# Kernel optimization log

Hardware: AMD Instinct MI355X
Metric: run time of the kernel (lower is better)

Reference implementation:

```python
import jax, jax.numpy as jnp
import numpy as np

B, C, H, W = 8, 256, 64, 64
G = min(C // 4, 32)  # 32 groups, as in the torch module
EPS = 1e-6


def setup_inputs() -> dict:
    key = jax.random.key(0)
    ks = jax.random.split(key, 12)
    s = 1.0 / np.sqrt(C)
    inp = {
        "x": jax.random.normal(ks[0], (B, C, H, W), jnp.float32),
        "gn_scale": 1.0 + 0.02 * jax.random.normal(ks[1], (C,), jnp.float32),
        "gn_bias": 0.02 * jax.random.normal(ks[2], (C,), jnp.float32),
        "w_q": s * jax.random.normal(ks[3], (C, C), jnp.float32),
        "b_q": 0.01 * jax.random.normal(ks[4], (C,), jnp.float32),
        "w_k": s * jax.random.normal(ks[5], (C, C), jnp.float32),
        "b_k": 0.01 * jax.random.normal(ks[6], (C,), jnp.float32),
        "w_v": s * jax.random.normal(ks[7], (C, C), jnp.float32),
        "b_v": 0.01 * jax.random.normal(ks[8], (C,), jnp.float32),
        "w_o": s * jax.random.normal(ks[9], (C, C), jnp.float32),
        "b_o": 0.01 * jax.random.normal(ks[10], (C,), jnp.float32),
    }
    return inp


def _group_norm(x, scale, bias):
    b, c, h, w = x.shape
    xg = x.reshape(b, G, c // G, h, w)
    m = jnp.mean(xg, axis=(2, 3, 4), keepdims=True)
    v = jnp.var(xg, axis=(2, 3, 4), keepdims=True)
    xn = ((xg - m) * jax.lax.rsqrt(v + EPS)).reshape(b, c, h, w)
    return xn * scale[None, :, None, None] + bias[None, :, None, None]


def _nin(h, w, b):
    # 1x1 conv: [B,C,H,W] x [out,in] -> [B,out,H,W]
    return jnp.einsum('bchw,oc->bohw', h, w) + b[None, :, None, None]


def reference(x, gn_scale, gn_bias, w_q, b_q, w_k, b_k, w_v, b_v, w_o, b_o):
    b, c, h, w = x.shape
    n = h * w
    hn = _group_norm(x, gn_scale, gn_bias)
    q = _nin(hn, w_q, b_q).reshape(b, c, n)
    k = _nin(hn, w_k, b_k).reshape(b, c, n)
    v = _nin(hn, w_v, b_v).reshape(b, c, n)
    scale = jnp.asarray(c, x.dtype) ** -0.5
    att = jax.nn.softmax(jnp.einsum('bcn,bcm->bnm', q, k) * scale, axis=-1)
    out = jnp.einsum('bnm,bcm->bcn', att, v).reshape(b, c, h, w)
    out = _nin(out, w_o, b_o)
    return (x + out) / jnp.asarray(np.sqrt(2.0), x.dtype)
```

## Files before the change

### kernel.cpp

```cpp
#include <hip/hip_runtime.h>

typedef __attribute__((ext_vector_type(8))) short bf16x8;
typedef __attribute__((ext_vector_type(4))) float f32x4;
typedef unsigned short us;

#define MFMA(a, b, c) __builtin_amdgcn_mfma_f32_16x16x32_bf16((a), (b), (c), 0, 0, 0)

__device__ __forceinline__ us f2bf(float f) {
  union { float f; unsigned int u; } x; x.f = f;
  return (us)((x.u + 0x7FFFu + ((x.u >> 16) & 1u)) >> 16);
}

__device__ __forceinline__ void glds16(const us* g, us* l) {
  __builtin_amdgcn_global_load_lds(
      (const __attribute__((address_space(1))) unsigned int*)g,
      (__attribute__((address_space(3))) unsigned int*)l, 16, 0, 0);
}

__global__ __launch_bounds__(256) void conv_w(const float* __restrict__ a, const float* __restrict__ b,
                                              const float* __restrict__ c, const float* __restrict__ d,
                                              us* __restrict__ oa, us* __restrict__ ob,
                                              us* __restrict__ oc, us* __restrict__ od) {
  int i = blockIdx.x * 256 + threadIdx.x;
  oa[i] = f2bf(a[i]); ob[i] = f2bf(b[i]); oc[i] = f2bf(c[i]); od[i] = f2bf(d[i]);
}

__global__ __launch_bounds__(256) void gn_kernel(const float* __restrict__ x,
                                                 const float* __restrict__ scale,
                                                 const float* __restrict__ bias,
                                                 us* __restrict__ hnT) {
  int b = blockIdx.y, g = blockIdx.x;
  int tid = threadIdx.x;
  int c0 = g * 8;
  const float* xb = x + (((size_t)b * 256 + c0) << 12);
  float s = 0.f, sq = 0.f;
  for (int j = 0; j < 8; ++j) {
    const float* xc = xb + ((size_t)j << 12);
    for (int n = tid; n < 4096; n += 256) {
      float v = xc[n];
      s += v; sq += v * v;
    }
  }
  for (int off = 32; off; off >>= 1) { s += __shfl_xor(s, off); sq += __shfl_xor(sq, off); }
  __shared__ float red[8];
  int w = tid >> 6, lane = tid & 63;
  if (lane == 0) { red[w] = s; red[4 + w] = sq; }
  __syncthreads();
  s  = red[0] + red[1] + red[2] + red[3];
  sq = red[4] + red[5] + red[6] + red[7];
  float mean = s * (1.f / 32768.f);
  float var  = sq * (1.f / 32768.f) - mean * mean;
  float rstd = rsqrtf(var + 1e-6f);
  float aa[8], bb[8];
  for (int j = 0; j < 8; ++j) {
    float sc = scale[c0 + j] * rstd;
    aa[j] = sc; bb[j] = bias[c0 + j] - mean * sc;
  }
  us* dst = hnT + ((size_t)b << 12) * 256 + c0;
  for (int n = tid; n < 4096; n += 256) {
    union { us u16[8]; uint4 v; } t;
    for (int j = 0; j < 8; ++j) {
      float v = xb[((size_t)j << 12) + n];
      t.u16[j] = f2bf(v * aa[j] + bb[j]);
    }
    *(uint4*)(dst + (size_t)n * 256) = t.v;
  }
}

__global__ __launch_bounds__(256) void proj_nk(const us* __restrict__ hnT,
                                               const us* __restrict__ wq, const us* __restrict__ wk,
                                               const float* __restrict__ bq, const float* __restrict__ bk,
                                               us* __restrict__ qT, us* __restrict__ kT) {
  __shared__ us A_s[128 * 64];
  __shared__ us B_s[128 * 64];
  int bx = blockIdx.x, by = blockIdx.y;
  int tid = threadIdx.x, w = tid >> 6, lane = tid & 63;
  int l15 = lane & 15, quad = lane >> 4;
  const us* wsrc; const float* bsrc; us* dst; int o0;
  if (by < 2) { wsrc = wq; bsrc = bq; dst = qT; o0 = by * 128; }
  else        { wsrc = wk; bsrc = bk; dst = kT; o0 = (by - 2) * 128; }
  size_t R0 = (size_t)bx * 128;
  int wm = (w & 1) * 64, wn = (w >> 1) * 64;
  f32x4 z = {0.f, 0.f, 0.f, 0.f};
  f32x4 acc[4][4] = {{z,z,z,z},{z,z,z,z},{z,z,z,z},{z,z,z,z}};

  for (int kk = 0; kk < 256; kk += 64) {
    __syncthreads();
#pragma unroll
    for (int j = 0; j < 4; ++j) {
      int cidx = j * 256 + tid;
      int row = cidx >> 3, cc = cidx & 7;
      int gch = (cc ^ (row & 7)) * 8;
      glds16(hnT + (R0 + row) * 256 + kk + gch, A_s + cidx * 8);
      glds16(wsrc + (size_t)(o0 + row) * 256 + kk + gch, B_s + cidx * 8);
    }
    __syncthreads();
#pragma unroll
    for (int k2 = 0; k2 < 2; ++k2) {
      int ch = (k2 * 4 + quad) ^ (l15 & 7);
      bf16x8 af[4], bf[4];
#pragma unroll
      for (int i = 0; i < 4; ++i) {
        af[i] = *(const bf16x8*)(A_s + (wm + i * 16 + l15) * 64 + ch * 8);
        bf[i] = *(const bf16x8*)(B_s + (wn + i * 16 + l15) * 64 + ch * 8);
      }
#pragma unroll
      for (int i = 0; i < 4; ++i)
#pragma unroll
        for (int j = 0; j < 4; ++j)
          acc[i][j] = MFMA(af[i], bf[j], acc[i][j]);
    }
  }
#pragma unroll
  for (int j = 0; j < 4; ++j) {
    int o = o0 + wn + j * 16 + l15;
    float bv = bsrc[o];
#pragma unroll
    for (int i = 0; i < 4; ++i)
#pragma unroll
      for (int r = 0; r < 4; ++r)
        dst[(R0 + wm + i * 16 + quad * 4 + r) * 256 + o] = f2bf(acc[i][j][r] + bv);
  }
}

__global__ __launch_bounds__(256) void proj_cn(const us* __restrict__ A,
                                               const us* __restrict__ Bm,
                                               const float* __restrict__ bias,
                                               const float* __restrict__ x,
                                               float* __restrict__ outf,
                                               us* __restrict__ outb, int mode) {
  __shared__ us A_s[128 * 64];
  __shared__ us B_s[128 * 64];
  int bx = blockIdx.x, bb = blockIdx.y;
  int mt = bx & 1, ntile = bx >> 1;
  int tid = threadIdx.x, w = tid >> 6, lane = tid & 63;
  int l15 = lane & 15, quad = lane >> 4;
  int R0 = mt * 128;
  size_t NB = (size_t)bb * 4096 + ntile * 128;
  int wm = (w & 1) * 64, wn = (w >> 1) * 64;
  f32x4 z = {0.f, 0.f, 0.f, 0.f};
  f32x4 acc[4][4] = {{z,z,z,z},{z,z,z,z},{z,z,z,z},{z,z,z,z}};

  for (int kk = 0; kk < 256; kk += 64) {
    __syncthreads();
#pragma unroll
    for (int j = 0; j < 4; ++j) {
      int cidx = j * 256 + tid;
      int row = cidx >> 3, cc = cidx & 7;
      int gch = (cc ^ (row & 7)) * 8;
      glds16(A + (size_t)(R0 + row) * 256 + kk + gch, A_s + cidx * 8);
      glds16(Bm + (NB + row) * 256 + kk + gch, B_s + cidx * 8);
    }
    __syncthreads();
#pragma unroll
    for (int k2 = 0; k2 < 2; ++k2) {
      int ch = (k2 * 4 + quad) ^ (l15 & 7);
      bf16x8 af[4], bf[4];
#pragma unroll
      for (int i = 0; i < 4; ++i) {
        af[i] = *(const bf16x8*)(A_s + (wm + i * 16 + l15) * 64 + ch * 8);
        bf[i] = *(const bf16x8*)(B_s + (wn + i * 16 + l15) * 64 + ch * 8);
      }
#pragma unroll
      for (int i = 0; i < 4; ++i)
#pragma unroll
        for (int j = 0; j < 4; ++j)
          acc[i][j] = MFMA(af[i], bf[j], acc[i][j]);
    }
  }
  const float is2 = 0.70710678118654752f;
#pragma unroll
  for (int i = 0; i < 4; ++i)
#pragma unroll
    for (int r = 0; r < 4; ++r) {
      int c = R0 + wm + i * 16 + quad * 4 + r;
      float bv = bias[c];
      size_t base = (((size_t)bb * 256 + c) << 12) + (ntile * 128 + wn);
      if (mode == 0) {
#pragma unroll
        for (int j = 0; j < 4; ++j)
          outb[base + j * 16 + l15] = f2bf(acc[i][j][r] + bv);
      } else {
#pragma unroll
        for (int j = 0; j < 4; ++j) {
          size_t idx = base + j * 16 + l15;
          outf[idx] = (x[idx] + acc[i][j][r] + bv) * is2;
        }
      }
    }
}

__global__ __launch_bounds__(512) void attn_partial(const us* __restrict__ qT,
                                                    const us* __restrict__ kT,
                                                    const us* __restrict__ vv,
                                                    float* __restrict__ Of,
                                                    us* __restrict__ Ob,
                                                    float* __restrict__ l0,
                                                    float* __restrict__ l1) {
  int b = blockIdx.y, nt = blockIdx.x, h = blockIdx.z;
  int tid = threadIdx.x, w = tid >> 6, lane = tid & 63;
  int l15 = lane & 15, quad = lane >> 4;
  __shared__ us kt_s[32 * 256];
  __shared__ us v_s[256 * 40];
  __shared__ us p_s[8][16 * 40];
  const us* qTb = qT + ((size_t)b << 12) * 256;
  const us* kTb = kT + ((size_t)b << 12) * 256;
  const us* vb  = vv + ((size_t)b << 12) * 256;
  int n0 = nt * 128 + w * 16;
  int m_base = h * 2048;
  bf16x8 qf[8];
#pragma unroll
  for (int ks = 0; ks < 8; ++ks)
    qf[ks] = *(const bf16x8*)(qTb + (size_t)(n0 + l15) * 256 + ks * 32 + quad * 8);
  f32x4 z = {0.f, 0.f, 0.f, 0.f};
  f32x4 of[16];
#pragma unroll
  for (int i = 0; i < 16; ++i) of[i] = z;
  float lrow[4] = {0.f, 0.f, 0.f, 0.f};

  int krow0 = tid >> 5, kch = tid & 31;
  int krow1 = krow0 + 16;
  int vrow0 = tid >> 2, vch = tid & 3;
  int vrow1 = vrow0 + 128;

  uint4 kr0 = *(const uint4*)(kTb + (size_t)(m_base + krow0) * 256 + kch * 8);
  uint4 kr1 = *(const uint4*)(kTb + (size_t)(m_base + krow1) * 256 + kch * 8);
  uint4 vr0 = *(const uint4*)(vb + ((size_t)vrow0 << 12) + m_base + vch * 8);
  uint4 vr1 = *(const uint4*)(vb + ((size_t)vrow1 << 12) + m_base + vch * 8);

  for (int mt = 0; mt < 64; ++mt) {
    __syncthreads();
    *(uint4*)(kt_s + krow0 * 256 + ((kch ^ (krow0 & 7)) * 8)) = kr0;
    *(uint4*)(kt_s + krow1 * 256 + ((kch ^ (krow1 & 7)) * 8)) = kr1;
    *(uint4*)(v_s + vrow0 * 40 + vch * 8) = vr0;
    *(uint4*)(v_s + vrow1 * 40 + vch * 8) = vr1;
    __syncthreads();
    if (mt < 63) {
      int m0n = m_base + (mt + 1) * 32;
      kr0 = *(const uint4*)(kTb + (size_t)(m0n + krow0) * 256 + kch * 8);
      kr1 = *(const uint4*)(kTb + (size_t)(m0n + krow1) * 256 + kch * 8);
      vr0 = *(const uint4*)(vb + ((size_t)vrow0 << 12) + m0n + vch * 8);
      vr1 = *(const uint4*)(vb + ((size_t)vrow1 << 12) + m0n + vch * 8);
    }

    f32x4 s0 = z, s1 = z;
#pragma unroll
    for (int ks = 0; ks < 8; ++ks) {
      int ch = ks * 4 + quad;
      int r0 = l15, r1 = 16 + l15;
      bf16x8 k0 = *(const bf16x8*)(kt_s + r0 * 256 + ((ch ^ (r0 & 7)) * 8));
      bf16x8 k1 = *(const bf16x8*)(kt_s + r1 * 256 + ((ch ^ (r1 & 7)) * 8));
      s0 = MFMA(qf[ks], k0, s0);
      s1 = MFMA(qf[ks], k1, s1);
    }

    const float sc = 0.0625f;
    us* pw = p_s[w];
#pragma unroll
    for (int r = 0; r < 4; ++r) {
      float p0 = __expf(s0[r] * sc);
      float p1 = __expf(s1[r] * sc);
      lrow[r] += p0 + p1;
      int n = quad * 4 + r;
      pw[n * 40 + l15]      = f2bf(p0);
      pw[n * 40 + 16 + l15] = f2bf(p1);
    }
    bf16x8 pf = *(const bf16x8*)(pw + l15 * 40 + quad * 8);
#pragma unroll
    for (int cs = 0; cs < 16; ++cs) {
      bf16x8 vf = *(const bf16x8*)(v_s + (cs * 16 + l15) * 40 + quad * 8);
      of[cs] = MFMA(pf, vf, of[cs]);
    }
  }

  size_t obase = ((size_t)b << 12) * 256;
#pragma unroll
  for (int r = 0; r < 4; ++r) {
    int n = n0 + quad * 4 + r;
    float l = lrow[r];
    l += __shfl_xor(l, 1);
    l += __shfl_xor(l, 2);
    l += __shfl_xor(l, 4);
    l += __shfl_xor(l, 8);
    size_t row = obase + (size_t)n * 256;
    if (h == 0) {
      if (l15 == 0) l0[((size_t)b << 12) + n] = l;
#pragma unroll
      for (int cs = 0; cs < 16; ++cs)
        Of[row + cs * 16 + l15] = of[cs][r];
    } else {
      if (l15 == 0) l1[((size_t)b << 12) + n] = l;
#pragma unroll
      for (int cs = 0; cs < 16; ++cs)
        Ob[row + cs * 16 + l15] = f2bf(of[cs][r]);
    }
  }
}

__global__ __launch_bounds__(256) void combine(const float* __restrict__ Of,
                                               const us* __restrict__ Ob,
                                               const float* __restrict__ l0,
                                               const float* __restrict__ l1,
                                               us* __restrict__ attT) {
  int idx = blockIdx.x * 256 + threadIdx.x;
  int row = idx >> 5;
  int c0 = (idx & 31) * 8;
  size_t base = (size_t)row * 256 + c0;
  float inv = 1.f / (l0[row] + l1[row]);
  float4 f0 = *(const float4*)(Of + base);
  float4 f1 = *(const float4*)(Of + base + 4);
  union { us u16[8]; uint4 v; } pb;
  pb.v = *(const uint4*)(Ob + base);
  union { us u16[8]; uint4 v; } t;
  float fo[8] = {f0.x, f0.y, f0.z, f0.w, f1.x, f1.y, f1.z, f1.w};
#pragma unroll
  for (int j = 0; j < 8; ++j) {
    union { unsigned int u; float f; } bu; bu.u = ((unsigned int)pb.u16[j]) << 16;
    t.u16[j] = f2bf((fo[j] + bu.f) * inv);
  }
  *(uint4*)(attT + base) = t.v;
}

extern "C" void kernel_launch(void* const* d_in, const int* in_sizes, int n_in,
                              void* d_out, int out_size, void* d_ws, size_t ws_size,
                              hipStream_t stream) {
  const float* x  = (const float*)d_in[0];
  const float* gs = (const float*)d_in[1];
  const float* gb = (const float*)d_in[2];
  const float* wq = (const float*)d_in[3];
  const float* bq = (const float*)d_in[4];
  const float* wk = (const float*)d_in[5];
  const float* bk = (const float*)d_in[6];
  const float* wv = (const float*)d_in[7];
  const float* bv = (const float*)d_in[8];
  const float* wo = (const float*)d_in[9];
  const float* bo = (const float*)d_in[10];
  float* out = (float*)d_out;

  us* ws = (us*)d_ws;
  const size_t SZ = (size_t)8 * 4096 * 256;
  us* hnT = ws;
  us* qT  = ws + SZ;
  us* kT  = ws + 2 * SZ;
  us* vvb = ws + 3 * SZ;
  us* wqb = ws + 4 * SZ;
  us* wkb = wqb + 65536;
  us* wvb = wkb + 65536;
  us* wob = wvb + 65536;
  float* l0 = (float*)(wob + 65536);
  float* l1 = l0 + 32768;
  float* Opart0 = out;
  us* Opart1 = hnT;
  us* attT = qT;

  conv_w<<<256, 256, 0, stream>>>(wq, wk, wv, wo, wqb, wkb, wvb, wob);
  gn_kernel<<<dim3(32, 8), 256, 0, stream>>>(x, gs, gb, hnT);
  proj_nk<<<dim3(256, 4), 256, 0, stream>>>(hnT, wqb, wkb, bq, bk, qT, kT);
  proj_cn<<<dim3(64, 8), 256, 0, stream>>>(wvb, hnT, bv, nullptr, nullptr, vvb, 0);
  attn_partial<<<dim3(32, 8, 2), 512, 0, stream>>>(qT, kT, vvb, Opart0, Opart1, l0, l1);
  combine<<<4096, 256, 0, stream>>>(Opart0, Opart1, l0, l1, attT);
  proj_cn<<<dim3(64, 8), 256, 0, stream>>>(wob, attT, bo, x, out, nullptr, 1);
}
```

Baseline: 436.5 us.

## Stream K tiles via direct global-to-LDS loads and read V fragments from global

In the attention kernel, K tiles are now loaded with global_load_lds into a padded, double-buffered LDS buffer, which removes the register staging and one barrier per iteration. V is no longer staged in LDS; each wave reads its V fragments straight from global memory right before the PV MFMAs. Launch bounds now request three blocks per CU, helped by the smaller LDS footprint. The cost is that every wave re-reads the full V tile from L2, and those loads sit on the critical path without prefetch. Completion of the async LDS loads also depends on the barrier waiting for outstanding memory operations.

New measurement: 964.5 us. +120.9%, slower.

```diff
diff --git a/kernel.cpp b/kernel.cpp
--- a/kernel.cpp
+++ b/kernel.cpp
@@ -190,18 +190,17 @@
     }
 }
 
-__global__ __launch_bounds__(512) void attn_partial(const us* __restrict__ qT,
-                                                    const us* __restrict__ kT,
-                                                    const us* __restrict__ vv,
-                                                    float* __restrict__ Of,
-                                                    us* __restrict__ Ob,
-                                                    float* __restrict__ l0,
-                                                    float* __restrict__ l1) {
+__global__ __launch_bounds__(512, 3) void attn_partial(const us* __restrict__ qT,
+                                                       const us* __restrict__ kT,
+                                                       const us* __restrict__ vv,
+                                                       float* __restrict__ Of,
+                                                       us* __restrict__ Ob,
+                                                       float* __restrict__ l0,
+                                                       float* __restrict__ l1) {
   int b = blockIdx.y, nt = blockIdx.x, h = blockIdx.z;
   int tid = threadIdx.x, w = tid >> 6, lane = tid & 63;
   int l15 = lane & 15, quad = lane >> 4;
-  __shared__ us kt_s[32 * 256];
-  __shared__ us v_s[256 * 40];
+  __shared__ us kt_s[2 * 16 * 520];
   __shared__ us p_s[8][16 * 40];
   const us* qTb = qT + ((size_t)b << 12) * 256;
   const us* kTb = kT + ((size_t)b << 12) * 256;
@@ -218,38 +217,34 @@
   for (int i = 0; i < 16; ++i) of[i] = z;
   float lrow[4] = {0.f, 0.f, 0.f, 0.f};
 
-  int krow0 = tid >> 5, kch = tid & 31;
-  int krow1 = krow0 + 16;
-  int vrow0 = tid >> 2, vch = tid & 3;
-  int vrow1 = vrow0 + 128;
-
-  uint4 kr0 = *(const uint4*)(kTb + (size_t)(m_base + krow0) * 256 + kch * 8);
-  uint4 kr1 = *(const uint4*)(kTb + (size_t)(m_base + krow1) * 256 + kch * 8);
-  uint4 vr0 = *(const uint4*)(vb + ((size_t)vrow0 << 12) + m_base + vch * 8);
-  uint4 vr1 = *(const uint4*)(vb + ((size_t)vrow1 << 12) + m_base + vch * 8);
+  int rA = 2 * w + (lane >> 5);
+  int rB = rA + 16;
+  int chs = (lane & 31) * 8;
+  us* dstA0 = kt_s + w * 520 + lane * 8;
+  us* dstB0 = kt_s + (8 + w) * 520 + lane * 8;
+
+  glds16(kTb + (size_t)(m_base + rA) * 256 + chs, dstA0);
+  glds16(kTb + (size_t)(m_base + rB) * 256 + chs, dstB0);
+  int cur = 0;
 
   for (int mt = 0; mt < 64; ++mt) {
     __syncthreads();
-    *(uint4*)(kt_s + krow0 * 256 + ((kch ^ (krow0 & 7)) * 8)) = kr0;
-    *(uint4*)(kt_s + krow1 * 256 + ((kch ^ (krow1 & 7)) * 8)) = kr1;
-    *(uint4*)(v_s + vrow0 * 40 + vch * 8) = vr0;
-    *(uint4*)(v_s + vrow1 * 40 + vch * 8) = vr1;
-    __syncthreads();
+    const us* kbuf = kt_s + cur * 8320;
     if (mt < 63) {
-      int m0n = m_base + (mt + 1) * 32;
-      kr0 = *(const uint4*)(kTb + (size_t)(m0n + krow0) * 256 + kch * 8);
-      kr1 = *(const uint4*)(kTb + (size_t)(m0n + krow1) * 256 + kch * 8);
-      vr0 = *(const uint4*)(vb + ((size_t)vrow0 << 12) + m0n + vch * 8);
-      vr1 = *(const uint4*)(vb + ((size_t)vrow1 << 12) + m0n + vch * 8);
+      int mn = m_base + (mt + 1) * 32;
+      us* da = kt_s + (cur ^ 1) * 8320;
+      glds16(kTb + (size_t)(mn + rA) * 256 + chs, da + w * 520 + lane * 8);
+      glds16(kTb + (size_t)(mn + rB) * 256 + chs, da + (8 + w) * 520 + lane * 8);
     }
 
     f32x4 s0 = z, s1 = z;
+    int roff0 = (l15 >> 1) * 520 + (l15 & 1) * 256;
+    int roff1 = roff0 + 8 * 520;
 #pragma unroll
     for (int ks = 0; ks < 8; ++ks) {
-      int ch = ks * 4 + quad;
-      int r0 = l15, r1 = 16 + l15;
-      bf16x8 k0 = *(const bf16x8*)(kt_s + r0 * 256 + ((ch ^ (r0 & 7)) * 8));
-      bf16x8 k1 = *(const bf16x8*)(kt_s + r1 * 256 + ((ch ^ (r1 & 7)) * 8));
+      int choff = (ks * 4 + quad) * 8;
+      bf16x8 k0 = *(const bf16x8*)(kbuf + roff0 + choff);
+      bf16x8 k1 = *(const bf16x8*)(kbuf + roff1 + choff);
       s0 = MFMA(qf[ks], k0, s0);
       s1 = MFMA(qf[ks], k1, s1);
     }
@@ -266,11 +261,19 @@
       pw[n * 40 + 16 + l15] = f2bf(p1);
     }
     bf16x8 pf = *(const bf16x8*)(pw + l15 * 40 + quad * 8);
-#pragma unroll
-    for (int cs = 0; cs < 16; ++cs) {
-      bf16x8 vf = *(const bf16x8*)(v_s + (cs * 16 + l15) * 40 + quad * 8);
-      of[cs] = MFMA(pf, vf, of[cs]);
-    }
+
+    int m0v = m_base + mt * 32;
+#pragma unroll
+    for (int g = 0; g < 4; ++g) {
+      bf16x8 vf[4];
+#pragma unroll
+      for (int u = 0; u < 4; ++u)
+        vf[u] = *(const bf16x8*)(vb + (((size_t)(g * 64 + u * 16 + l15)) << 12) + m0v + quad * 8);
+#pragma unroll
+      for (int u = 0; u < 4; ++u)
+        of[g * 4 + u] = MFMA(pf, vf[u], of[g * 4 + u]);
+    }
+    cur ^= 1;
   }
 
   size_t obase = ((size_t)b << 12) * 256;
```

## Switch attention Q/K/V and probabilities to FP8 MFMA with smaller blocks

Applied to the files above, without the earlier changes.

Q, K and V projections now emit FP8 (e4m3) instead of bf16, and the attention kernel uses the fp8 16x16x32 MFMA for both the QK^T and PV products, with the softmax probabilities packed to FP8. This halves the bytes streamed for K/V tiles and LDS traffic. Blocks shrink from 512 to 256 threads with twice as many blocks. Scores are clamped before exp so FP8 does not overflow, which together with the reduced precision risks accuracy loss.

After: 428.8 us. No clear change (-1.8%).

```diff
diff --git a/kernel.cpp b/kernel.cpp
--- a/kernel.cpp
+++ b/kernel.cpp
@@ -3,12 +3,18 @@
 typedef __attribute__((ext_vector_type(8))) short bf16x8;
 typedef __attribute__((ext_vector_type(4))) float f32x4;
 typedef unsigned short us;
+typedef unsigned char u8;
+typedef long i64;
 
 #define MFMA(a, b, c) __builtin_amdgcn_mfma_f32_16x16x32_bf16((a), (b), (c), 0, 0, 0)
+#define MFMA8(a, b, c) __builtin_amdgcn_mfma_f32_16x16x32_fp8_fp8((a), (b), (c), 0, 0, 0)
 
 __device__ __forceinline__ us f2bf(float f) {
   union { float f; unsigned int u; } x; x.f = f;
   return (us)((x.u + 0x7FFFu + ((x.u >> 16) & 1u)) >> 16);
+}
+__device__ __forceinline__ u8 f2fp8(float f) {
+  return (u8)(__builtin_amdgcn_cvt_pk_fp8_f32(f, f, 0, false) & 0xFF);
 }
 
 __device__ __forceinline__ void glds16(const us* g, us* l) {
@@ -70,15 +76,15 @@
 __global__ __launch_bounds__(256) void proj_nk(const us* __restrict__ hnT,
                                                const us* __restrict__ wq, const us* __restrict__ wk,
                                                const float* __restrict__ bq, const float* __restrict__ bk,
-                                               us* __restrict__ qT, us* __restrict__ kT) {
+                                               u8* __restrict__ q8, u8* __restrict__ k8) {
   __shared__ us A_s[128 * 64];
   __shared__ us B_s[128 * 64];
   int bx = blockIdx.x, by = blockIdx.y;
   int tid = threadIdx.x, w = tid >> 6, lane = tid & 63;
   int l15 = lane & 15, quad = lane >> 4;
-  const us* wsrc; const float* bsrc; us* dst; int o0;
-  if (by < 2) { wsrc = wq; bsrc = bq; dst = qT; o0 = by * 128; }
-  else        { wsrc = wk; bsrc = bk; dst = kT; o0 = (by - 2) * 128; }
+  const us* wsrc; const float* bsrc; u8* dst; int o0;
+  if (by < 2) { wsrc = wq; bsrc = bq; dst = q8; o0 = by * 128; }
+  else        { wsrc = wk; bsrc = bk; dst = k8; o0 = (by - 2) * 128; }
   size_t R0 = (size_t)bx * 128;
   int wm = (w & 1) * 64, wn = (w >> 1) * 64;
   f32x4 z = {0.f, 0.f, 0.f, 0.f};
@@ -119,7 +125,7 @@
     for (int i = 0; i < 4; ++i)
 #pragma unroll
       for (int r = 0; r < 4; ++r)
-        dst[(R0 + wm + i * 16 + quad * 4 + r) * 256 + o] = f2bf(acc[i][j][r] + bv);
+        dst[(R0 + wm + i * 16 + quad * 4 + r) * 256 + o] = f2fp8(acc[i][j][r] + bv);
   }
 }
 
@@ -128,7 +134,7 @@
                                                const float* __restrict__ bias,
                                                const float* __restrict__ x,
                                                float* __restrict__ outf,
-                                               us* __restrict__ outb, int mode) {
+                                               u8* __restrict__ out8, int mode) {
   __shared__ us A_s[128 * 64];
   __shared__ us B_s[128 * 64];
   int bx = blockIdx.x, bb = blockIdx.y;
@@ -179,7 +185,7 @@
       if (mode == 0) {
 #pragma unroll
         for (int j = 0; j < 4; ++j)
-          outb[base + j * 16 + l15] = f2bf(acc[i][j][r] + bv);
+          out8[base + j * 16 + l15] = f2fp8(acc[i][j][r] + bv);
       } else {
 #pragma unroll
         for (int j = 0; j < 4; ++j) {
@@ -190,9 +196,9 @@
     }
 }
 
-__global__ __launch_bounds__(512) void attn_partial(const us* __restrict__ qT,
-                                                    const us* __restrict__ kT,
-                                                    const us* __restrict__ vv,
+__global__ __launch_bounds__(256) void attn_partial(const u8* __restrict__ q8,
+                                                    const u8* __restrict__ k8,
+                                                    const u8* __restrict__ v8,
                                                     float* __restrict__ Of,
                                                     us* __restrict__ Ob,
                                                     float* __restrict__ l0,
@@ -200,76 +206,78 @@
   int b = blockIdx.y, nt = blockIdx.x, h = blockIdx.z;
   int tid = threadIdx.x, w = tid >> 6, lane = tid & 63;
   int l15 = lane & 15, quad = lane >> 4;
-  __shared__ us kt_s[32 * 256];
-  __shared__ us v_s[256 * 40];
-  __shared__ us p_s[8][16 * 40];
-  const us* qTb = qT + ((size_t)b << 12) * 256;
-  const us* kTb = kT + ((size_t)b << 12) * 256;
-  const us* vb  = vv + ((size_t)b << 12) * 256;
-  int n0 = nt * 128 + w * 16;
+  __shared__ u8 kt_s[32 * 256];
+  __shared__ u8 v_s[256 * 48];
+  __shared__ u8 p_s[4 * 16 * 40];
+  const u8* qb = q8 + ((size_t)b << 12) * 256;
+  const u8* kb = k8 + ((size_t)b << 12) * 256;
+  const u8* vb = v8 + ((size_t)b << 12) * 256;
+  int n0 = nt * 64 + w * 16;
   int m_base = h * 2048;
-  bf16x8 qf[8];
+  i64 qf[8];
 #pragma unroll
   for (int ks = 0; ks < 8; ++ks)
-    qf[ks] = *(const bf16x8*)(qTb + (size_t)(n0 + l15) * 256 + ks * 32 + quad * 8);
+    qf[ks] = *(const i64*)(qb + (size_t)(n0 + l15) * 256 + ks * 32 + quad * 8);
   f32x4 z = {0.f, 0.f, 0.f, 0.f};
   f32x4 of[16];
 #pragma unroll
   for (int i = 0; i < 16; ++i) of[i] = z;
   float lrow[4] = {0.f, 0.f, 0.f, 0.f};
 
-  int krow0 = tid >> 5, kch = tid & 31;
-  int krow1 = krow0 + 16;
-  int vrow0 = tid >> 2, vch = tid & 3;
-  int vrow1 = vrow0 + 128;
-
-  uint4 kr0 = *(const uint4*)(kTb + (size_t)(m_base + krow0) * 256 + kch * 8);
-  uint4 kr1 = *(const uint4*)(kTb + (size_t)(m_base + krow1) * 256 + kch * 8);
-  uint4 vr0 = *(const uint4*)(vb + ((size_t)vrow0 << 12) + m_base + vch * 8);
-  uint4 vr1 = *(const uint4*)(vb + ((size_t)vrow1 << 12) + m_base + vch * 8);
+  int km = tid >> 4, kj = tid & 15;
+  int km2 = km + 16;
+  int ksw = (kj ^ (km & 15)) * 16;
+  int vc = tid;
+
+  uint4 kr0 = *(const uint4*)(kb + (size_t)(m_base + km) * 256 + kj * 16);
+  uint4 kr1 = *(const uint4*)(kb + (size_t)(m_base + km2) * 256 + kj * 16);
+  uint4 vr0 = *(const uint4*)(vb + ((size_t)vc << 12) + m_base);
+  uint4 vr1 = *(const uint4*)(vb + ((size_t)vc << 12) + m_base + 16);
 
   for (int mt = 0; mt < 64; ++mt) {
     __syncthreads();
-    *(uint4*)(kt_s + krow0 * 256 + ((kch ^ (krow0 & 7)) * 8)) = kr0;
-    *(uint4*)(kt_s + krow1 * 256 + ((kch ^ (krow1 & 7)) * 8)) = kr1;
-    *(uint4*)(v_s + vrow0 * 40 + vch * 8) = vr0;
-    *(uint4*)(v_s + vrow1 * 40 + vch * 8) = vr1;
+    *(uint4*)(kt_s + km * 256 + ksw) = kr0;
+    *(uint4*)(kt_s + km2 * 256 + ksw) = kr1;
+    *(uint4*)(v_s + vc * 48) = vr0;
+    *(uint4*)(v_s + vc * 48 + 16) = vr1;
     __syncthreads();
     if (mt < 63) {
-      int m0n = m_base + (mt + 1) * 32;
-      kr0 = *(const uint4*)(kTb + (size_t)(m0n + krow0) * 256 + kch * 8);
-      kr1 = *(const uint4*)(kTb + (size_t)(m0n + krow1) * 256 + kch * 8);
-      vr0 = *(const uint4*)(vb + ((size_t)vrow0 << 12) + m0n + vch * 8);
-      vr1 = *(const uint4*)(vb + ((size_t)vrow1 << 12) + m0n + vch * 8);
+      int mn = m_base + (mt + 1) * 32;
+      kr0 = *(const uint4*)(kb + (size_t)(mn + km) * 256 + kj * 16);
+      kr1 = *(const uint4*)(kb + (size_t)(mn + km2) * 256 + kj * 16);
+      vr0 = *(const uint4*)(vb + ((size_t)vc << 12) + mn);
+      vr1 = *(const uint4*)(vb + ((size_t)vc << 12) + mn + 16);
     }
 
     f32x4 s0 = z, s1 = z;
+    int r0 = l15, r1 = 16 + l15;
 #pragma unroll
     for (int ks = 0; ks < 8; ++ks) {
-      int ch = ks * 4 + quad;
-      int r0 = l15, r1 = 16 + l15;
-      bf16x8 k0 = *(const bf16x8*)(kt_s + r0 * 256 + ((ch ^ (r0 & 7)) * 8));
-      bf16x8 k1 = *(const bf16x8*)(kt_s + r1 * 256 + ((ch ^ (r1 & 7)) * 8));
-      s0 = MFMA(qf[ks], k0, s0);
-      s1 = MFMA(qf[ks], k1, s1);
+      int ch = ks * 2 + (quad >> 1), half = (quad & 1) * 8;
+      i64 k0 = *(const i64*)(kt_s + r0 * 256 + ((ch ^ (r0 & 15)) * 16) + half);
+      i64 k1 = *(const i64*)(kt_s + r1 * 256 + ((ch ^ (r1 & 15)) * 16) + half);
+      s0 = MFMA8(qf[ks], k0, s0);
+      s1 = MFMA8(qf[ks], k1, s1);
     }
 
     const float sc = 0.0625f;
-    us* pw = p_s[w];
+    u8* pw = p_s + w * 640;
 #pragma unroll
     for (int r = 0; r < 4; ++r) {
-      float p0 = __expf(s0[r] * sc);
-      float p1 = __expf(s1[r] * sc);
+      float p0 = __expf(fminf(s0[r] * sc, 5.9f));
+      float p1 = __expf(fminf(s1[r] * sc, 5.9f));
       lrow[r] += p0 + p1;
+      int pk = __builtin_amdgcn_cvt_pk_fp8_f32(p0, p1, 0, false);
       int n = quad * 4 + r;
-      pw[n * 40 + l15]      = f2bf(p0);
-      pw[n * 40 + 16 + l15] = f2bf(p1);
-    }
-    bf16x8 pf = *(const bf16x8*)(pw + l15 * 40 + quad * 8);
+      pw[n * 40 + l15]      = (u8)(pk & 0xFF);
+      pw[n * 40 + 16 + l15] = (u8)((pk >> 8) & 0xFF);
+    }
+    i64 pf = *(const i64*)(pw + l15 * 40 + quad * 8);
+
 #pragma unroll
     for (int cs = 0; cs < 16; ++cs) {
-      bf16x8 vf = *(const bf16x8*)(v_s + (cs * 16 + l15) * 40 + quad * 8);
-      of[cs] = MFMA(pf, vf, of[cs]);
+      i64 vf = *(const i64*)(v_s + (cs * 16 + l15) * 48 + quad * 8);
+      of[cs] = MFMA8(pf, vf, of[cs]);
     }
   }
 
@@ -340,10 +348,10 @@
   us* ws = (us*)d_ws;
   const size_t SZ = (size_t)8 * 4096 * 256;
   us* hnT = ws;
-  us* qT  = ws + SZ;
-  us* kT  = ws + 2 * SZ;
-  us* vvb = ws + 3 * SZ;
-  us* wqb = ws + 4 * SZ;
+  u8* q8  = (u8*)(ws + SZ);
+  u8* k8  = q8 + SZ;
+  u8* v8  = k8 + SZ;
+  us* wqb = (us*)(v8 + SZ);
   us* wkb = wqb + 65536;
   us* wvb = wkb + 65536;
   us* wob = wvb + 65536;
@@ -351,13 +359,13 @@
   float* l1 = l0 + 32768;
   float* Opart0 = out;
   us* Opart1 = hnT;
-  us* attT = qT;
+  us* attT = (us*)q8;
 
   conv_w<<<256, 256, 0, stream>>>(wq, wk, wv, wo, wqb, wkb, wvb, wob);
   gn_kernel<<<dim3(32, 8), 256, 0, stream>>>(x, gs, gb, hnT);
-  proj_nk<<<dim3(256, 4), 256, 0, stream>>>(hnT, wqb, wkb, bq, bk, qT, kT);
-  proj_cn<<<dim3(64, 8), 256, 0, stream>>>(wvb, hnT, bv, nullptr, nullptr, vvb, 0);
-  attn_partial<<<dim3(32, 8, 2), 512, 0, stream>>>(qT, kT, vvb, Opart0, Opart1, l0, l1);
+  proj_nk<<<dim3(256, 4), 256, 0, stream>>>(hnT, wqb, wkb, bq, bk, q8, k8);
+  proj_cn<<<dim3(64, 8), 256, 0, stream>>>(wvb, hnT, bv, nullptr, nullptr, v8, 0);
+  attn_partial<<<dim3(64, 8, 2), 256, 0, stream>>>(q8, k8, v8, Opart0, Opart1, l0, l1);
   combine<<<4096, 256, 0, stream>>>(Opart0, Opart1, l0, l1, attT);
   proj_cn<<<dim3(64, 8), 256, 0, stream>>>(wob, attT, bo, x, out, nullptr, 1);
 }
```
